# Kernel optimization log

Measured on AMD Instinct MI355X. Metric: run time of the kernel, lower is better.

## Reference

```python
import jax, jax.numpy as jnp
import numpy as np

# Tree config: batch of perfect binary trees in heap layout (root=0, children of i are 2i+1, 2i+2)
D_MODEL = 512
DEPTH = 10                      # number of internal levels
B = 64                          # number of trees in the batch
VOCAB = 32000
N_LEAVES = 2 ** DEPTH           # 1024 leaves per tree
N_NODES = 2 ** (DEPTH + 1) - 1  # 2047 nodes per tree
N_CLASSES = 2                   # binary graph classification


def setup_inputs() -> dict:
    key = jax.random.key(0)
    k_tok, k_emb, k_iou, k_f, k_out = jax.random.split(key, 5)
    d = D_MODEL
    s_in = 1.0 / np.sqrt(2 * d)
    return {
        "tokens": jax.random.randint(k_tok, (B, N_LEAVES), 0, VOCAB, dtype=jnp.int32),
        "embedding": (jax.random.normal(k_emb, (VOCAB, d), jnp.float32) * 0.02),
        "W_iou": jax.random.normal(k_iou, (2 * d, 3 * d), jnp.float32) * s_in,
        "b_iou": jnp.zeros((3 * d,), jnp.float32),
        "W_f": jax.random.normal(k_f, (2 * d, 2 * d), jnp.float32) * s_in,
        "b_f": jnp.zeros((2 * d,), jnp.float32),
        "W_out": jax.random.normal(k_out, (d, N_CLASSES), jnp.float32) * (1.0 / np.sqrt(d)),
    }


def reference(tokens, embedding, W_iou, b_iou, W_f, b_f, W_out):
    # Shared activation / memory buffers over all nodes, as in RecursiveNN.forward.
    d = embedding.shape[1]
    b = tokens.shape[0]
    h = jnp.zeros((b, N_NODES, d), jnp.float32)   # activations
    c = jnp.zeros((b, N_NODES, d), jnp.float32)   # memory (memory_size=1)

    # Leaves: embedding lookup, scattered into the activation buffer.
    leaf_h = embedding[tokens]                    # [B, N_LEAVES, d]
    h = h.at[:, N_LEAVES - 1:].set(leaf_h)

    # Internal nodes by topological level (leaf-adjacent level first, root last).
    for level in range(DEPTH - 1, -1, -1):
        idx = np.arange(2 ** level - 1, 2 ** (level + 1) - 1)  # node group (static)
        left, right = 2 * idx + 1, 2 * idx + 2                 # predecessor indices
        # Gather predecessor activations and memory.
        hl, hr = h[:, left], h[:, right]                       # [B, n, d]
        cl, cr = c[:, left], c[:, right]
        x = jnp.concatenate([hl, hr], axis=-1)                 # [B, n, 2d]
        # Binary TreeLSTM cell (the _apply_function for the 'add' binary op).
        iou = x @ W_iou + b_iou
        i, o, u = jnp.split(iou, 3, axis=-1)
        f = jax.nn.sigmoid(x @ W_f + b_f)
        fl, fr = jnp.split(f, 2, axis=-1)
        c_new = jax.nn.sigmoid(i) * jnp.tanh(u) + fl * cl + fr * cr
        h_new = jax.nn.sigmoid(o) * jnp.tanh(c_new)
        # Scatter back into the shared buffers.
        h = h.at[:, idx].set(h_new)
        c = c.at[:, idx].set(c_new)

    # _compute_output: linear binary-classification head on the root activation.
    return h[:, 0] @ W_out                                     # [B, N_CLASSES]
```

## Files before the change

### kernel.cpp

```cpp
#include <hip/hip_runtime.h>
#include <math.h>

typedef unsigned short u16;
typedef short s16x8 __attribute__((ext_vector_type(8)));
typedef float f32x4 __attribute__((ext_vector_type(4)));

#define NITER 32
#define ARW 72

__device__ __align__(16) u16 g_Bhi[1024 * 2560];
__device__ __align__(16) u16 g_Blo[1024 * 2560];
__device__ __align__(16) u16 g_Aleaf[(size_t)64 * 1024 * 1024];

__device__ __forceinline__ u16 f2bf(float x) {
    unsigned u = __float_as_uint(x);
    u += 0x7fffu + ((u >> 16) & 1u);
    return (u16)(u >> 16);
}
__device__ __forceinline__ float bf2f(u16 h) { return __uint_as_float(((unsigned)h) << 16); }
__device__ __forceinline__ float sigm(float x) { return 1.0f / (1.0f + expf(-x)); }
__device__ __forceinline__ unsigned pk(u16 a, u16 b) { return (unsigned)a | ((unsigned)b << 16); }

__device__ __forceinline__ void gload16(const void* g, u16* l) {
    __builtin_amdgcn_global_load_lds(
        (const __attribute__((address_space(1))) void*)g,
        (__attribute__((address_space(3))) void*)(void*)l, 16, 0, 0);
}

__global__ __launch_bounds__(256)
void wsplit_kernel(const float* __restrict__ Wiou, const float* __restrict__ Wf)
{
    __shared__ float tile[32][65];
    const int kb = blockIdx.x;
    const int cb = blockIdx.y;
    const int t  = threadIdx.x;
    const int c0 = cb * 64;

    {
        const int kk  = t >> 3;
        const int cu0 = (t & 7) * 8;
        const int k   = kb * 32 + kk;
#pragma unroll
        for (int u = 0; u < 8; u++) {
            int c = c0 + cu0 + u;
            float v = (c < 1536) ? Wiou[(size_t)k * 1536 + c]
                                 : Wf[(size_t)k * 1024 + (c - 1536)];
            tile[kk][cu0 + u] = v;
        }
    }
    __syncthreads();
    {
        const int jl = t >> 2;
        const int kc = (t & 3) * 8;
        const int g  = c0 >> 9;
        const int j  = (c0 & 511) + jl;
        size_t dst = (((size_t)kb * 5 + g) * 512 + j) * 32 + kc;
        unsigned ph[4], pl[4];
#pragma unroll
        for (int u = 0; u < 4; u++) {
            float v0 = tile[kc + 2 * u][jl];
            float v1 = tile[kc + 2 * u + 1][jl];
            u16 h0 = f2bf(v0), h1 = f2bf(v1);
            u16 l0 = f2bf(v0 - bf2f(h0)), l1 = f2bf(v1 - bf2f(h1));
            ph[u] = pk(h0, h1);
            pl[u] = pk(l0, l1);
        }
        *(uint4*)(g_Bhi + dst) = make_uint4(ph[0], ph[1], ph[2], ph[3]);
        *(uint4*)(g_Blo + dst) = make_uint4(pl[0], pl[1], pl[2], pl[3]);
    }
}

__global__ __launch_bounds__(256)
void leafgather_kernel(const int* __restrict__ tokens, const float* __restrict__ emb)
{
    const int gidx = blockIdx.x * 256 + threadIdx.x;
    const int row  = gidx >> 5;
    const int c    = gidx & 31;
    const int tok  = tokens[row];
    const float* src = emb + (size_t)tok * 512 + c * 16;
    u16* dst = g_Aleaf + (size_t)row * 1024 + c * 32;

    float4 f0 = *(const float4*)(src);
    float4 f1 = *(const float4*)(src + 4);
    float4 f2 = *(const float4*)(src + 8);
    float4 f3 = *(const float4*)(src + 12);
    float v[16] = {f0.x,f0.y,f0.z,f0.w, f1.x,f1.y,f1.z,f1.w,
                   f2.x,f2.y,f2.z,f2.w, f3.x,f3.y,f3.z,f3.w};
    unsigned ph[8], pl[8];
#pragma unroll
    for (int i = 0; i < 8; i++) {
        u16 h0 = f2bf(v[2*i]),   h1 = f2bf(v[2*i+1]);
        u16 l0 = f2bf(v[2*i]   - bf2f(h0));
        u16 l1 = f2bf(v[2*i+1] - bf2f(h1));
        ph[i] = pk(h0, h1);
        pl[i] = pk(l0, l1);
    }
    *(uint4*)(dst)      = make_uint4(ph[0], ph[1], ph[2], ph[3]);
    *(uint4*)(dst + 8)  = make_uint4(ph[4], ph[5], ph[6], ph[7]);
    *(uint4*)(dst + 16) = make_uint4(pl[0], pl[1], pl[2], pl[3]);
    *(uint4*)(dst + 24) = make_uint4(pl[4], pl[5], pl[6], pl[7]);
}

template<bool LEAF>
__global__ __launch_bounds__(256, 2)
void level_big(const u16* __restrict__ Hcin, const float* __restrict__ Cc,
               const float* __restrict__ b_iou, const float* __restrict__ b_f,
               u16* __restrict__ Hp, float* __restrict__ Cp,
               int np, int lgnp)
{
    __shared__ __align__(16) u16 Ab0[8192];
    __shared__ __align__(16) u16 Ab1[8192];

    const u16* Hc = LEAF ? g_Aleaf : Hcin;

    const int tid = threadIdx.x;
    const int jg  = blockIdx.x;
    const int m0  = blockIdx.y * 64;
    const int j0  = jg * 64;
    const int nc  = np * 2;

    const int w    = tid >> 6;
    const int lane = tid & 63;
    const int il   = lane & 15;
    const int kq   = lane >> 4;
    const int wc   = w;

    f32x4 acc[4][5];
#pragma unroll
    for (int rf = 0; rf < 4; rf++)
#pragma unroll
        for (int g = 0; g < 5; g++) acc[rf][g] = (f32x4)0.0f;

    const int bA  = m0 >> lgnp;
    const int pA0 = m0 & (np - 1);
    const char* A0u = (const char*)(Hc + ((size_t)bA * nc + 2 * pA0) * 1024);
    const int rowS = tid >> 3;
    const int segS = (tid & 7) ^ (rowS & 7);
    const unsigned voffA = (unsigned)rowS * 4096u + (unsigned)segS * 16u;

    const int shi = ((kq >> 1) << 2) | (kq & 1);
    const int x7  = il & 7;
    const int aoh = il * 64 + ((shi ^ x7) * 8);
    const int aol = il * 64 + (((shi + 2) ^ x7) * 8);

    const char* BH0 = (const char*)(g_Bhi + (size_t)j0 * 32);
    const char* BL0 = (const char*)(g_Blo + (size_t)j0 * 32);
    unsigned vB[5];
#pragma unroll
    for (int g = 0; g < 5; g++)
        vB[g] = (unsigned)(((wc * 16 + il) * 32 + kq * 8) * 2 + g * 32768);

    s16x8 bh[5], bl[5];

#define STAGEA2(DST, t_)                                                       \
    {                                                                          \
        const char* ab = A0u + (size_t)(t_) * 128;                             \
        gload16(ab + voffA, (DST) + w * 512);                                  \
        gload16(ab + 131072 + voffA, (DST) + 2048 + w * 512);                  \
    }

#define LOADB_HI(t_)                                                           \
    {                                                                          \
        const char* bhp = BH0 + (size_t)(t_) * 163840;                         \
        _Pragma("unroll")                                                      \
        for (int g = 0; g < 5; g++) bh[g] = *(const s16x8*)(bhp + vB[g]);      \
    }

#define LOADB_LO(t_)                                                           \
    {                                                                          \
        const char* blp = BL0 + (size_t)(t_) * 163840;                         \
        _Pragma("unroll")                                                      \
        for (int g = 0; g < 5; g++) bl[g] = *(const s16x8*)(blp + vB[g]);      \
    }

#define MFMA_PASS(AREGS, BSET)                                                 \
    {                                                                          \
        __builtin_amdgcn_s_setprio(1);                                         \
        _Pragma("unroll")                                                      \
        for (int rf = 0; rf < 4; rf++)                                         \
            _Pragma("unroll")                                                  \
            for (int g = 0; g < 5; g++)                                        \
                acc[rf][g] = __builtin_amdgcn_mfma_f32_16x16x32_bf16(AREGS[rf], BSET[g], acc[rf][g], 0, 0, 0); \
        __builtin_amdgcn_s_setprio(0);                                         \
    }

#define TILE_COMPUTE(ABASE, tload_, do_load_)                                  \
    {                                                                          \
        s16x8 ah[4], al[4];                                                    \
        _Pragma("unroll")                                                      \
        for (int rf = 0; rf < 4; rf++) {                                       \
            ah[rf] = *(const s16x8*)&(ABASE)[aoh + rf * 1024];                 \
            al[rf] = *(const s16x8*)&(ABASE)[aol + rf * 1024];                 \
        }                                                                      \
        MFMA_PASS(ah, bh);                                                     \
        MFMA_PASS(al, bh);                                                     \
        if (do_load_) LOADB_HI(tload_);                                        \
        MFMA_PASS(ah, bl);                                                     \
        if (do_load_) LOADB_LO(tload_);                                        \
    }

#define WINDOW(ACUR, ANXT, t0_, more_)                                         \
    {                                                                          \
        if (more_) {                                                           \
            STAGEA2(ANXT, (t0_) + 2);                                          \
            STAGEA2((ANXT) + 4096, (t0_) + 3);                                 \
            __builtin_amdgcn_sched_barrier(0);                                 \
        }                                                                      \
        TILE_COMPUTE(ACUR, (t0_) + 1, 1);                                      \
        TILE_COMPUTE((ACUR) + 4096, (t0_) + 2, more_);                         \
        if (more_) {                                                           \
            asm volatile("s_waitcnt vmcnt(10)" ::: "memory");                  \
            __builtin_amdgcn_s_barrier();                                      \
            __builtin_amdgcn_sched_barrier(0);                                 \
        }                                                                      \
    }

    STAGEA2(Ab0, 0);
    STAGEA2(Ab0 + 4096, 1);
    __builtin_amdgcn_sched_barrier(0);
    LOADB_HI(0);
    LOADB_LO(0);
    asm volatile("s_waitcnt vmcnt(10)" ::: "memory");
    __builtin_amdgcn_s_barrier();
    __builtin_amdgcn_sched_barrier(0);

#pragma unroll 1
    for (int t0 = 0; t0 < NITER; t0 += 4) {
        WINDOW(Ab0, Ab1, t0, 1);
        WINDOW(Ab1, Ab0, t0 + 2, (t0 + 4 < NITER));
    }
#undef STAGEA2
#undef LOADB_HI
#undef LOADB_LO
#undef MFMA_PASS
#undef TILE_COMPUTE
#undef WINDOW

    const int jglob = j0 + wc * 16 + il;
    const float bi  = b_iou[jglob];
    const float bo_ = b_iou[512 + jglob];
    const float bu  = b_iou[1024 + jglob];
    const float bfl = b_f[jglob];
    const float bfr = b_f[512 + jglob];

#pragma unroll
    for (int rf = 0; rf < 4; rf++) {
#pragma unroll
        for (int r = 0; r < 4; r++) {
            const int m  = m0 + rf * 16 + kq * 4 + r;
            const int b  = m >> lgnp;
            const int p  = m & (np - 1);
            float i_ = acc[rf][0][r] + bi;
            float o_ = acc[rf][1][r] + bo_;
            float u_ = acc[rf][2][r] + bu;
            float fl = sigm(acc[rf][3][r] + bfl);
            float fr = sigm(acc[rf][4][r] + bfr);
            float cl = 0.0f, cr_ = 0.0f;
            if (!LEAF) {
                size_t cb_ = ((size_t)b * nc + 2 * p) * 512 + jglob;
                cl  = Cc[cb_];
                cr_ = Cc[cb_ + 512];
            }
            float cn = sigm(i_) * tanhf(u_) + fl * cl + fr * cr_;
            float hn = sigm(o_) * tanhf(cn);
            size_t prow = (size_t)b * np + p;
            u16 hh  = f2bf(hn);
            u16 hlo = f2bf(hn - bf2f(hh));
            Hp[prow * 1024 + (size_t)(jg * 4 + wc) * 32 + il]      = hh;
            Hp[prow * 1024 + (size_t)(jg * 4 + wc) * 32 + 16 + il] = hlo;
            Cp[prow * 512 + jglob] = cn;
        }
    }
}

__global__ __launch_bounds__(256, 2)
void level_small(const u16* __restrict__ Hc, const float* __restrict__ Cc,
                 const float* __restrict__ b_iou, const float* __restrict__ b_f,
                 u16* __restrict__ Hp, float* __restrict__ Cp,
                 int np, int lgnp)
{
    __shared__ __align__(16) u16 Ac[2][64 * ARW];

    const int tid = threadIdx.x;
    const int jg  = blockIdx.x;
    const int m0  = blockIdx.y * 64;
    const int j0  = jg * 64;
    const int nc  = np * 2;
    const int M   = np * 64;

    const int w    = tid >> 6;
    const int lane = tid & 63;
    const int il   = lane & 15;
    const int kq   = lane >> 4;
    const int wc   = w;

    f32x4 acc[4][5];
#pragma unroll
    for (int rf = 0; rf < 4; rf++)
#pragma unroll
        for (int g = 0; g < 5; g++) acc[rf][g] = (f32x4)0.0f;

    const int rA = tid >> 2;
    const int qA = tid & 3;
    int mA = m0 + rA; if (mA > M - 1) mA = M - 1;
    const int bA = mA >> lgnp;
    const int pA = mA & (np - 1);
    const u16* arow = Hc + ((size_t)bA * nc + 2 * pA) * 1024;
    const int daI = rA * ARW + (qA & 1) * 32 + (qA >> 1) * 16;

    const char* BH0 = (const char*)(g_Bhi + (size_t)j0 * 32);
    const char* BL0 = (const char*)(g_Blo + (size_t)j0 * 32);
    unsigned vB[5];
#pragma unroll
    for (int g = 0; g < 5; g++)
        vB[g] = (unsigned)(((wc * 16 + il) * 32 + kq * 8) * 2 + g * 32768);

    uint4  aR0, aR1;
    s16x8 b0h[5], b0l[5], b1h[5], b1l[5];

#define LOADA(t_)                                                              \
    {                                                                          \
        const u16* asrc = arow + (t_) * 64 + qA * 16;                          \
        aR0 = *(const uint4*)asrc;                                             \
        aR1 = *(const uint4*)(asrc + 8);                                       \
    }
#define LOADB(BH, BL, t_)                                                      \
    {                                                                          \
        const char* bh = BH0 + (size_t)(t_) * 163840;                          \
        const char* bl = BL0 + (size_t)(t_) * 163840;                          \
        _Pragma("unroll")                                                      \
        for (int g = 0; g < 5; g++) {                                          \
            BH[g] = *(const s16x8*)(bh + vB[g]);                               \
            BL[g] = *(const s16x8*)(bl + vB[g]);                               \
        }                                                                      \
    }
#define WRITEA(bf)                                                             \
    {                                                                          \
        *(uint4*)&Ac[bf][daI]     = aR0;                                       \
        *(uint4*)&Ac[bf][daI + 8] = aR1;                                       \
    }
#define COMPUTE(BH, BL, BUF)                                                   \
    {                                                                          \
        _Pragma("unroll")                                                      \
        for (int rf = 0; rf < 4; rf++) {                                       \
            const int ao = (rf * 16 + il) * ARW + kq * 8;                      \
            s16x8 ahv = *(const s16x8*)&Ac[BUF][ao];                           \
            s16x8 alv = *(const s16x8*)&Ac[BUF][ao + 32];                      \
            _Pragma("unroll")                                                  \
            for (int g = 0; g < 5; g++) {                                      \
                acc[rf][g] = __builtin_amdgcn_mfma_f32_16x16x32_bf16(ahv, BH[g], acc[rf][g], 0, 0, 0); \
                acc[rf][g] = __builtin_amdgcn_mfma_f32_16x16x32_bf16(ahv, BL[g], acc[rf][g], 0, 0, 0); \
                acc[rf][g] = __builtin_amdgcn_mfma_f32_16x16x32_bf16(alv, BH[g], acc[rf][g], 0, 0, 0); \
            }                                                                  \
        }                                                                      \
    }

    LOADA(0);
    LOADB(b0h, b0l, 0);
    WRITEA(0);
    __syncthreads();

#pragma unroll 1
    for (int t = 0; t < NITER; t += 2) {
        if (t + 1 < NITER) { LOADA(t + 1); LOADB(b1h, b1l, t + 1); }
        COMPUTE(b0h, b0l, 0);
        if (t + 1 < NITER) { WRITEA(1); __syncthreads(); }
        if (t + 2 < NITER) { LOADA(t + 2); LOADB(b0h, b0l, t + 2); }
        COMPUTE(b1h, b1l, 1);
        if (t + 2 < NITER) { WRITEA(0); __syncthreads(); }
    }
#undef LOADA
#undef LOADB
#undef WRITEA
#undef COMPUTE

    const int jglob = j0 + wc * 16 + il;
    const float bi  = b_iou[jglob];
    const float bo_ = b_iou[512 + jglob];
    const float bu  = b_iou[1024 + jglob];
    const float bfl = b_f[jglob];
    const float bfr = b_f[512 + jglob];

#pragma unroll
    for (int rf = 0; rf < 4; rf++) {
#pragma unroll
        for (int r = 0; r < 4; r++) {
            const int m = m0 + rf * 16 + kq * 4 + r;
            if (m < M) {
                const int b = m >> lgnp;
                const int p = m & (np - 1);
                float i_ = acc[rf][0][r] + bi;
                float o_ = acc[rf][1][r] + bo_;
                float u_ = acc[rf][2][r] + bu;
                float fl = sigm(acc[rf][3][r] + bfl);
                float fr = sigm(acc[rf][4][r] + bfr);
                size_t cb_ = ((size_t)b * nc + 2 * p) * 512 + jglob;
                float cl  = Cc[cb_];
                float cr_ = Cc[cb_ + 512];
                float cn = sigm(i_) * tanhf(u_) + fl * cl + fr * cr_;
                float hn = sigm(o_) * tanhf(cn);
                size_t prow = (size_t)b * np + p;
                u16 hh  = f2bf(hn);
                u16 hlo = f2bf(hn - bf2f(hh));
                Hp[prow * 1024 + (size_t)(jg * 4 + wc) * 32 + il]      = hh;
                Hp[prow * 1024 + (size_t)(jg * 4 + wc) * 32 + 16 + il] = hlo;
                Cp[prow * 512 + jglob] = cn;
            }
        }
    }
}

__global__ __launch_bounds__(256)
void out_kernel(const u16* __restrict__ Hroot, const float* __restrict__ W_out,
                float* __restrict__ out)
{
    const int b = blockIdx.x;
    const int tid = threadIdx.x;
    float s0 = 0.f, s1 = 0.f;
    for (int d = tid; d < 512; d += 256) {
        const u16* row = Hroot + (size_t)b * 1024 + (d >> 4) * 32 + (d & 15);
        float h = bf2f(row[0]) + bf2f(row[16]);
        s0 = fmaf(h, W_out[d * 2 + 0], s0);
        s1 = fmaf(h, W_out[d * 2 + 1], s1);
    }
#pragma unroll
    for (int off = 32; off > 0; off >>= 1) {
        s0 += __shfl_down(s0, off, 64);
        s1 += __shfl_down(s1, off, 64);
    }
    __shared__ float red[2][4];
    const int wave = tid >> 6;
    if ((tid & 63) == 0) { red[0][wave] = s0; red[1][wave] = s1; }
    __syncthreads();
    if (tid == 0) {
        float t0 = 0.f, t1 = 0.f;
#pragma unroll
        for (int wv = 0; wv < 4; wv++) { t0 += red[0][wv]; t1 += red[1][wv]; }
        out[b * 2 + 0] = t0;
        out[b * 2 + 1] = t1;
    }
}

extern "C" void kernel_launch(void* const* d_in, const int* in_sizes, int n_in,
                              void* d_out, int out_size, void* d_ws, size_t ws_size,
                              hipStream_t stream)
{
    const int*   tokens = (const int*)  d_in[0];
    const float* emb    = (const float*)d_in[1];
    const float* W_iou  = (const float*)d_in[2];
    const float* b_iou  = (const float*)d_in[3];
    const float* W_f    = (const float*)d_in[4];
    const float* b_f    = (const float*)d_in[5];
    const float* W_out  = (const float*)d_in[6];
    float* out = (float*)d_out;

    u16*   H0 = (u16*)d_ws;
    float* C0 = (float*)(H0 + (size_t)512 * 64 * 1024);
    u16*   H1 = (u16*)(C0 + (size_t)512 * 64 * 512);
    float* C1 = (float*)(H1 + (size_t)256 * 64 * 1024);

    wsplit_kernel<<<dim3(32, 40), 256, 0, stream>>>(W_iou, W_f);
    leafgather_kernel<<<8192, 256, 0, stream>>>(tokens, emb);

    level_big<true><<<dim3(8, 512), 256, 0, stream>>>(
        nullptr, nullptr, b_iou, b_f, H0, C0, 512, 9);

    u16* Hc = H0;  float* Cc = C0;
    u16* Hp = H1;  float* Cp = C1;
    for (int L = 8; L >= 0; L--) {
        const int np = 1 << L;
        if (np >= 64) {
            level_big<false><<<dim3(8, np), 256, 0, stream>>>(
                Hc, Cc, b_iou, b_f, Hp, Cp, np, L);
        } else {
            level_small<<<dim3(8, np), 256, 0, stream>>>(
                Hc, Cc, b_iou, b_f, Hp, Cp, np, L);
        }
        u16* tH = Hc; Hc = Hp; Hp = tH;
        float* tC = Cc; Cc = Cp; Cp = tC;
    }

    out_kernel<<<64, 256, 0, stream>>>(Hc, W_out, out);
}
```

Measured before the change: 1.237 ms.

## Double-buffer B fragments and prefetch A fragments across MFMA passes

Splits the B-operand registers into two sets so loads for the next tile go into one set while MFMAs consume the other. A-fragment LDS reads for the next tile are moved ahead of and between MFMA passes instead of happening at the start of each tile. The goal is to hide global and LDS load latency behind matrix-core work. In exchange it raises VGPR pressure, which could reduce occupancy or cause spills, and the initial A read after the barrier adds a dependency at the start of each window.

```diff
diff --git a/kernel.cpp b/kernel.cpp
--- a/kernel.cpp
+++ b/kernel.cpp
@@ -150,7 +150,8 @@
     for (int g = 0; g < 5; g++)
         vB[g] = (unsigned)(((wc * 16 + il) * 32 + kq * 8) * 2 + g * 32768);
 
-    s16x8 bh[5], bl[5];
+    s16x8 b0h[5], b0l[5], b1h[5], b1l[5];
+    s16x8 ah[4], al[4], ahn[4];
 
 #define STAGEA2(DST, t_)                                                       \
     {                                                                          \
@@ -159,18 +160,32 @@
         gload16(ab + 131072 + voffA, (DST) + 2048 + w * 512);                  \
     }
 
-#define LOADB_HI(t_)                                                           \
+#define LOADB_HI(BH, t_)                                                       \
     {                                                                          \
         const char* bhp = BH0 + (size_t)(t_) * 163840;                         \
         _Pragma("unroll")                                                      \
-        for (int g = 0; g < 5; g++) bh[g] = *(const s16x8*)(bhp + vB[g]);      \
-    }
-
-#define LOADB_LO(t_)                                                           \
+        for (int g = 0; g < 5; g++) BH[g] = *(const s16x8*)(bhp + vB[g]);      \
+    }
+
+#define LOADB_LO(BL, t_)                                                       \
     {                                                                          \
         const char* blp = BL0 + (size_t)(t_) * 163840;                         \
         _Pragma("unroll")                                                      \
-        for (int g = 0; g < 5; g++) bl[g] = *(const s16x8*)(blp + vB[g]);      \
+        for (int g = 0; g < 5; g++) BL[g] = *(const s16x8*)(blp + vB[g]);      \
+    }
+
+#define READ_AH(DST, ABASE)                                                    \
+    {                                                                          \
+        _Pragma("unroll")                                                      \
+        for (int rf = 0; rf < 4; rf++)                                         \
+            DST[rf] = *(const s16x8*)&(ABASE)[aoh + rf * 1024];                \
+    }
+
+#define READ_AL(DST, ABASE)                                                    \
+    {                                                                          \
+        _Pragma("unroll")                                                      \
+        for (int rf = 0; rf < 4; rf++)                                         \
+            DST[rf] = *(const s16x8*)&(ABASE)[aol + rf * 1024];                \
     }
 
 #define MFMA_PASS(AREGS, BSET)                                                 \
@@ -184,21 +199,6 @@
         __builtin_amdgcn_s_setprio(0);                                         \
     }
 
-#define TILE_COMPUTE(ABASE, tload_, do_load_)                                  \
-    {                                                                          \
-        s16x8 ah[4], al[4];                                                    \
-        _Pragma("unroll")                                                      \
-        for (int rf = 0; rf < 4; rf++) {                                       \
-            ah[rf] = *(const s16x8*)&(ABASE)[aoh + rf * 1024];                 \
-            al[rf] = *(const s16x8*)&(ABASE)[aol + rf * 1024];                 \
-        }                                                                      \
-        MFMA_PASS(ah, bh);                                                     \
-        MFMA_PASS(al, bh);                                                     \
-        if (do_load_) LOADB_HI(tload_);                                        \
-        MFMA_PASS(ah, bl);                                                     \
-        if (do_load_) LOADB_LO(tload_);                                        \
-    }
-
 #define WINDOW(ACUR, ANXT, t0_, more_)                                         \
     {                                                                          \
         if (more_) {                                                           \
@@ -206,23 +206,39 @@
             STAGEA2((ANXT) + 4096, (t0_) + 3);                                 \
             __builtin_amdgcn_sched_barrier(0);                                 \
         }                                                                      \
-        TILE_COMPUTE(ACUR, (t0_) + 1, 1);                                      \
-        TILE_COMPUTE((ACUR) + 4096, (t0_) + 2, more_);                         \
+                                                             \
+        MFMA_PASS(ah, b0h);                                                    \
+        LOADB_HI(b1h, (t0_) + 1);                                              \
+        MFMA_PASS(al, b0h);                                                    \
+        LOADB_LO(b1l, (t0_) + 1);                                              \
+        READ_AH(ahn, (ACUR) + 4096);           \
+        MFMA_PASS(ah, b0l);                                                    \
+                                                             \
+        READ_AL(al, (ACUR) + 4096);            \
+        MFMA_PASS(ahn, b1h);                                                   \
+        if (more_) LOADB_HI(b0h, (t0_) + 2);                                   \
+        MFMA_PASS(al, b1h);                                                    \
+        if (more_) LOADB_LO(b0l, (t0_) + 2);                                   \
+        MFMA_PASS(ahn, b1l);                                                   \
         if (more_) {                                                           \
             asm volatile("s_waitcnt vmcnt(10)" ::: "memory");                  \
             __builtin_amdgcn_s_barrier();                                      \
             __builtin_amdgcn_sched_barrier(0);                                 \
+            READ_AH(ah, ANXT);                       \
+            READ_AL(al, ANXT);                                                 \
         }                                                                      \
     }
 
     STAGEA2(Ab0, 0);
     STAGEA2(Ab0 + 4096, 1);
     __builtin_amdgcn_sched_barrier(0);
-    LOADB_HI(0);
-    LOADB_LO(0);
+    LOADB_HI(b0h, 0);
+    LOADB_LO(b0l, 0);
     asm volatile("s_waitcnt vmcnt(10)" ::: "memory");
     __builtin_amdgcn_s_barrier();
     __builtin_amdgcn_sched_barrier(0);
+    READ_AH(ah, Ab0);
+    READ_AL(al, Ab0);
 
 #pragma unroll 1
     for (int t0 = 0; t0 < NITER; t0 += 4) {
@@ -232,8 +248,9 @@
 #undef STAGEA2
 #undef LOADB_HI
 #undef LOADB_LO
+#undef READ_AH
+#undef READ_AL
 #undef MFMA_PASS
-#undef TILE_COMPUTE
 #undef WINDOW
 
     const int jglob = j0 + wc * 16 + il;
```

After: 1.649 ms. 1.33x slower.
